# Performance work log

Measured on AMD Instinct MI355X. Metric: run time of the kernel, lower is better.

Reference implementation:

```python
import jax, jax.numpy as jnp
import numpy as np

B, M, K, N = 4, 2048, 4096, 4096


def setup_inputs() -> dict:
    key = jax.random.key(0)
    k1, k2, k3, k4, k5 = jax.random.split(key, 5)
    # quantized activations in [-8, 7], stored as int8 (spec dtype int32, cast here)
    x_q = jax.random.randint(k1, (B, M, K), -8, 8, dtype=jnp.int32).astype(jnp.int8)
    # per-token activation scales (B, M, 1)
    scales_x = jax.random.uniform(k2, (B, M, 1), dtype=jnp.float32, minval=0.001, maxval=0.02)
    # int8 weight (N, K) in [-8, 7] as produced by from_float
    weight = jax.random.randint(k3, (N, K), -8, 8, dtype=jnp.int32).astype(jnp.int8)
    # per-output-row weight scales (N, 1)
    weight_scales = jax.random.uniform(k4, (N, 1), dtype=jnp.float32, minval=0.001, maxval=0.02)
    bias = jax.random.normal(k5, (N,), dtype=jnp.float32) * 0.02
    return {"x_q": x_q, "scales_x": scales_x, "weight": weight,
            "weight_scales": weight_scales, "bias": bias}


def reference(x_q, scales_x, weight, weight_scales, bias):
    acc = jnp.einsum('bmk,nk->bmn', x_q, weight,
                     preferred_element_type=jnp.int32)  # (B, M, N) int32
    # sym_dequant: per-token scale * per-row weight scale, then fused bias add
    out = acc.astype(jnp.float32) * scales_x * weight_scales.reshape(1, 1, N) + bias
    return out
```

## Files before the change

### kernel.cpp

```cpp
#include <hip/hip_runtime.h>
#include <stdint.h>

#define MROWS 8192
#define K_DIM 4096
#define N_DIM 4096
#define BM 256
#define BN 256
#define BK 64
#define KT (K_DIM / BK)
#define ABYTES (BM * BK)
#define TBYTES (2 * ABYTES)

#define X_ELEMS (MROWS * K_DIM)
#define W_ELEMS (N_DIM * K_DIM)

typedef __attribute__((ext_vector_type(4))) int   int4v;
typedef __attribute__((ext_vector_type(4))) float float4v;

#define GLOAD_LDS16(gptr, lptr)                                                   \
    __builtin_amdgcn_global_load_lds((const __attribute__((address_space(1))) void*)(gptr), \
                                     (__attribute__((address_space(3))) void*)(lptr), 16, 0, 0)

__device__ __forceinline__ int pack4(int4v v) {
    return (int)((unsigned)(v[0] & 0xFF)
               | ((unsigned)(v[1] & 0xFF) << 8)
               | ((unsigned)(v[2] & 0xFF) << 16)
               | ((unsigned)(v[3] & 0xFF) << 24));
}

__global__ __launch_bounds__(256) void pack_i32_to_i8(
    const int4v* __restrict__ src, int4v* __restrict__ dst, int n16)
{
    int i = blockIdx.x * blockDim.x + threadIdx.x;
    if (i >= n16) return;
    int4v a = src[4 * i + 0];
    int4v b = src[4 * i + 1];
    int4v c = src[4 * i + 2];
    int4v d = src[4 * i + 3];
    int4v r;
    r[0] = pack4(a); r[1] = pack4(b); r[2] = pack4(c); r[3] = pack4(d);
    dst[i] = r;
}

__global__ __launch_bounds__(512, 2) void i8gemm_dq_kernel(
    const int8_t* __restrict__ xq,
    const float*  __restrict__ sx,
    const int8_t* __restrict__ wt,
    const float*  __restrict__ ws,
    const float*  __restrict__ bias,
    float*        __restrict__ out)
{
    __shared__ __align__(16) int8_t lds8[4 * TBYTES];

    const int tid  = threadIdx.x;
    const int wave = tid >> 6;
    const int lane = tid & 63;
    const int wr   = wave >> 2;
    const int wcn  = wave & 3;

    const int bid = blockIdx.x;
    const int wg  = (bid & 7) * 64 + (bid >> 3);
    const int ct  = wg & 15;
    const int rt  = wg >> 4;

    const int srow = wave * 16 + (lane >> 2);
    const int scol = (((lane & 3) - ((lane >> 3) & 3)) & 3) * 16;
    const int8_t* gA0 = xq + (size_t)(rt * BM + srow) * K_DIM + scol;
    const int8_t* gA1 = gA0 + (size_t)128 * K_DIM;
    const int8_t* gB0 = wt + (size_t)(ct * BN + srow) * K_DIM + scol;
    const int8_t* gB1 = gB0 + (size_t)128 * K_DIM;
    const int dA0 = wave * 1024;
    const int dA1 = 8192 + wave * 1024;
    const int dB0 = ABYTES + wave * 1024;
    const int dB1 = ABYTES + 8192 + wave * 1024;

    const int mrow = lane & 15;
    const int kswz = (((lane >> 4) + (mrow >> 1)) & 3) * 16;
    const int aoff = (wr * 128 + mrow) * BK + kswz;
    const int boff = ABYTES + (wcn * 64 + mrow) * BK + kswz;

    int4v acc[8][4] = {};

    #pragma unroll
    for (int u = 0; u < 3; ++u) {
        const size_t ko = (size_t)u * BK;
        int8_t* bb = lds8 + u * TBYTES;
        GLOAD_LDS16(gA0 + ko, bb + dA0);
        GLOAD_LDS16(gA1 + ko, bb + dA1);
        GLOAD_LDS16(gB0 + ko, bb + dB0);
        GLOAD_LDS16(gB1 + ko, bb + dB1);
    }

    #pragma unroll 4
    for (int t = 0; t < KT; ++t) {
        const int  buf = t & 3;
        const int  nb  = (t + 3) & 3;
        const int  u   = (t + 3) & (KT - 1);
        const size_t ko = (size_t)u * BK;
        const int8_t* base = lds8 + buf * TBYTES;
        int8_t* nbb = lds8 + nb * TBYTES;

        asm volatile("s_waitcnt vmcnt(8)" ::: "memory");
        __builtin_amdgcn_s_barrier();
        __builtin_amdgcn_sched_barrier(0);

        int4v a[4], b[4];
        #pragma unroll
        for (int i = 0; i < 4; ++i) a[i] = *(const int4v*)(base + aoff + i * 1024);
        #pragma unroll
        for (int j = 0; j < 4; ++j) b[j] = *(const int4v*)(base + boff + j * 1024);
        GLOAD_LDS16(gA0 + ko, nbb + dA0);
        GLOAD_LDS16(gA1 + ko, nbb + dA1);

        __builtin_amdgcn_s_setprio(1);
        #pragma unroll
        for (int i = 0; i < 4; ++i)
            #pragma unroll
            for (int j = 0; j < 4; ++j)
                acc[i][j] = __builtin_amdgcn_mfma_i32_16x16x64_i8(
                                a[i], b[j], acc[i][j], 0, 0, 0);
        __builtin_amdgcn_s_setprio(0);

        int4v a2[4];
        #pragma unroll
        for (int i = 0; i < 4; ++i) a2[i] = *(const int4v*)(base + aoff + (4 + i) * 1024);
        GLOAD_LDS16(gB0 + ko, nbb + dB0);
        GLOAD_LDS16(gB1 + ko, nbb + dB1);

        __builtin_amdgcn_s_setprio(1);
        #pragma unroll
        for (int i = 0; i < 4; ++i)
            #pragma unroll
            for (int j = 0; j < 4; ++j)
                acc[4 + i][j] = __builtin_amdgcn_mfma_i32_16x16x64_i8(
                                    a2[i], b[j], acc[4 + i][j], 0, 0, 0);
        __builtin_amdgcn_s_setprio(0);
    }

    asm volatile("s_waitcnt vmcnt(0)" ::: "memory");

    const int row_base = rt * BM + wr * 128;
    const int col_base = ct * BN + wcn * 64;
    const int crow = (lane >> 4) * 4;
    const int ccol = lane & 15;

    float wsc[4], bsc[4];
    #pragma unroll
    for (int j = 0; j < 4; ++j) {
        const int c = col_base + j * 16 + ccol;
        wsc[j] = ws[c];
        bsc[j] = bias[c];
    }

    #pragma unroll
    for (int i = 0; i < 8; ++i) {
        const int r0 = row_base + i * 16 + crow;
        const float4v sx4 = *(const float4v*)(sx + r0);
        #pragma unroll
        for (int j = 0; j < 4; ++j) {
            const int c = col_base + j * 16 + ccol;
            float* o = out + (size_t)r0 * N_DIM + c;
            #pragma unroll
            for (int r = 0; r < 4; ++r)
                o[(size_t)r * N_DIM] = (float)acc[i][j][r] * sx4[r] * wsc[j] + bsc[j];
        }
    }
}

extern "C" void kernel_launch(void* const* d_in, const int* in_sizes, int n_in,
                              void* d_out, int out_size, void* d_ws, size_t ws_size,
                              hipStream_t stream) {
    const int*   xq32 = (const int*)d_in[0];
    const float* sx   = (const float*)d_in[1];
    const int*   wt32 = (const int*)d_in[2];
    const float* ws   = (const float*)d_in[3];
    const float* bias = (const float*)d_in[4];
    float* out = (float*)d_out;

    int8_t* xq8 = (int8_t*)d_ws;
    int8_t* wt8 = xq8 + (size_t)X_ELEMS;

    {
        int n16x = X_ELEMS / 16;
        int n16w = W_ELEMS / 16;
        pack_i32_to_i8<<<n16x / 256, 256, 0, stream>>>((const int4v*)xq32, (int4v*)xq8, n16x);
        pack_i32_to_i8<<<n16w / 256, 256, 0, stream>>>((const int4v*)wt32, (int4v*)wt8, n16w);
    }

    dim3 grid((MROWS / BM) * (N_DIM / BN));
    i8gemm_dq_kernel<<<grid, 512, 0, stream>>>(xq8, sx, wt8, ws, bias, out);
}
```

Before: 396.4 us.

## Shrink GEMM tile to 256x128 with 4 waves and triple-buffered LDS

Halves the N tile to 128 and the workgroup to 4 waves, so the grid doubles and each wave keeps its 128x64 accumulator footprint. The LDS pipeline goes from 4 slots with 3 tiles in flight to 3 slots with 2 in flight. The loop now stops issuing prefetches for the last two K tiles, which are handled in a separate epilogue instead of wrapping around. The intent is smaller LDS use and better occupancy and load balance across CUs, at the cost of less reuse of A per workgroup and a shallower prefetch depth.

Result: slower. 410.0 us (+3.4%).

```diff
diff --git a/kernel.cpp b/kernel.cpp
--- a/kernel.cpp
+++ b/kernel.cpp
@@ -5,11 +5,12 @@
 #define K_DIM 4096
 #define N_DIM 4096
 #define BM 256
-#define BN 256
+#define BN 128
 #define BK 64
 #define KT (K_DIM / BK)
-#define ABYTES (BM * BK)
-#define TBYTES (2 * ABYTES)
+#define A_BYTES (BM * BK)
+#define B_BYTES (BN * BK)
+#define SLOT (A_BYTES + B_BYTES)
 
 #define X_ELEMS (MROWS * K_DIM)
 #define W_ELEMS (N_DIM * K_DIM)
@@ -42,7 +43,7 @@
     dst[i] = r;
 }
 
-__global__ __launch_bounds__(512, 2) void i8gemm_dq_kernel(
+__global__ __launch_bounds__(256, 2) void i8gemm_dq_kernel(
     const int8_t* __restrict__ xq,
     const float*  __restrict__ sx,
     const int8_t* __restrict__ wt,
@@ -50,57 +51,59 @@
     const float*  __restrict__ bias,
     float*        __restrict__ out)
 {
-    __shared__ __align__(16) int8_t lds8[4 * TBYTES];
+    __shared__ __align__(16) int8_t lds8[3 * SLOT];
 
     const int tid  = threadIdx.x;
     const int wave = tid >> 6;
     const int lane = tid & 63;
-    const int wr   = wave >> 2;
-    const int wcn  = wave & 3;
+    const int wrow = wave >> 1;
+    const int wcol = wave & 1;
 
     const int bid = blockIdx.x;
-    const int wg  = (bid & 7) * 64 + (bid >> 3);
-    const int ct  = wg & 15;
-    const int rt  = wg >> 4;
+    const int wg  = (bid & 7) * 128 + (bid >> 3);
+    const int ct  = wg & 31;
+    const int rt  = wg >> 5;
 
     const int srow = wave * 16 + (lane >> 2);
     const int scol = (((lane & 3) - ((lane >> 3) & 3)) & 3) * 16;
-    const int8_t* gA0 = xq + (size_t)(rt * BM + srow) * K_DIM + scol;
-    const int8_t* gA1 = gA0 + (size_t)128 * K_DIM;
-    const int8_t* gB0 = wt + (size_t)(ct * BN + srow) * K_DIM + scol;
-    const int8_t* gB1 = gB0 + (size_t)128 * K_DIM;
-    const int dA0 = wave * 1024;
-    const int dA1 = 8192 + wave * 1024;
-    const int dB0 = ABYTES + wave * 1024;
-    const int dB1 = ABYTES + 8192 + wave * 1024;
+    const int8_t* gA = xq + (size_t)(rt * BM + srow) * K_DIM + scol;
+    const int8_t* gB = wt + (size_t)(ct * BN + srow) * K_DIM + scol;
+    const int dA = wave * 1024;
+    const int dB = A_BYTES + wave * 1024;
 
     const int mrow = lane & 15;
     const int kswz = (((lane >> 4) + (mrow >> 1)) & 3) * 16;
-    const int aoff = (wr * 128 + mrow) * BK + kswz;
-    const int boff = ABYTES + (wcn * 64 + mrow) * BK + kswz;
+    const int aoff = (wrow * 128 + mrow) * BK + kswz;
+    const int boff = A_BYTES + (wcol * 64 + mrow) * BK + kswz;
 
     int4v acc[8][4] = {};
 
-    #pragma unroll
-    for (int u = 0; u < 3; ++u) {
-        const size_t ko = (size_t)u * BK;
-        int8_t* bb = lds8 + u * TBYTES;
-        GLOAD_LDS16(gA0 + ko, bb + dA0);
-        GLOAD_LDS16(gA1 + ko, bb + dA1);
-        GLOAD_LDS16(gB0 + ko, bb + dB0);
-        GLOAD_LDS16(gB1 + ko, bb + dB1);
-    }
-
-    #pragma unroll 4
-    for (int t = 0; t < KT; ++t) {
-        const int  buf = t & 3;
-        const int  nb  = (t + 3) & 3;
-        const int  u   = (t + 3) & (KT - 1);
-        const size_t ko = (size_t)u * BK;
-        const int8_t* base = lds8 + buf * TBYTES;
-        int8_t* nbb = lds8 + nb * TBYTES;
-
-        asm volatile("s_waitcnt vmcnt(8)" ::: "memory");
+#define STAGE_A012(U, S)                                       \
+    {                                                          \
+        const size_t ko_ = (size_t)(U) * BK;                   \
+        int8_t* bb_ = lds8 + (S) * SLOT;                       \
+        GLOAD_LDS16(gA + ko_,                   bb_ + dA);     \
+        GLOAD_LDS16(gA +  64 * K_DIM + ko_, bb_ + dA + 4096);  \
+        GLOAD_LDS16(gA + 128 * K_DIM + ko_, bb_ + dA + 8192);  \
+    }
+#define STAGE_A3B(U, S)                                        \
+    {                                                          \
+        const size_t ko_ = (size_t)(U) * BK;                   \
+        int8_t* bb_ = lds8 + (S) * SLOT;                       \
+        GLOAD_LDS16(gA + 192 * K_DIM + ko_, bb_ + dA + 12288); \
+        GLOAD_LDS16(gB + ko_,                   bb_ + dB);     \
+        GLOAD_LDS16(gB +  64 * K_DIM + ko_, bb_ + dB + 4096);  \
+    }
+
+    STAGE_A012(0, 0); STAGE_A3B(0, 0);
+    STAGE_A012(1, 1); STAGE_A3B(1, 1);
+
+    #pragma unroll 3
+    for (int t = 0; t < KT - 2; ++t) {
+        const int8_t* base = lds8 + (t % 3) * SLOT;
+        const int s2 = (t + 2) % 3;
+
+        asm volatile("s_waitcnt vmcnt(6)" ::: "memory");
         __builtin_amdgcn_s_barrier();
         __builtin_amdgcn_sched_barrier(0);
 
@@ -109,8 +112,7 @@
         for (int i = 0; i < 4; ++i) a[i] = *(const int4v*)(base + aoff + i * 1024);
         #pragma unroll
         for (int j = 0; j < 4; ++j) b[j] = *(const int4v*)(base + boff + j * 1024);
-        GLOAD_LDS16(gA0 + ko, nbb + dA0);
-        GLOAD_LDS16(gA1 + ko, nbb + dA1);
+        STAGE_A012(t + 2, s2);
 
         __builtin_amdgcn_s_setprio(1);
         #pragma unroll
@@ -124,8 +126,7 @@
         int4v a2[4];
         #pragma unroll
         for (int i = 0; i < 4; ++i) a2[i] = *(const int4v*)(base + aoff + (4 + i) * 1024);
-        GLOAD_LDS16(gB0 + ko, nbb + dB0);
-        GLOAD_LDS16(gB1 + ko, nbb + dB1);
+        STAGE_A3B(t + 2, s2);
 
         __builtin_amdgcn_s_setprio(1);
         #pragma unroll
@@ -137,10 +138,42 @@
         __builtin_amdgcn_s_setprio(0);
     }
 
-    asm volatile("s_waitcnt vmcnt(0)" ::: "memory");
-
-    const int row_base = rt * BM + wr * 128;
-    const int col_base = ct * BN + wcn * 64;
+    #pragma unroll
+    for (int e = 0; e < 2; ++e) {
+        const int t = KT - 2 + e;
+        const int8_t* base = lds8 + (t % 3) * SLOT;
+        if (e == 0) asm volatile("s_waitcnt vmcnt(6)" ::: "memory");
+        else        asm volatile("s_waitcnt vmcnt(0)" ::: "memory");
+        __builtin_amdgcn_s_barrier();
+        __builtin_amdgcn_sched_barrier(0);
+        int4v a[4], b[4], a2[4];
+        #pragma unroll
+        for (int i = 0; i < 4; ++i) a[i]  = *(const int4v*)(base + aoff + i * 1024);
+        #pragma unroll
+        for (int j = 0; j < 4; ++j) b[j]  = *(const int4v*)(base + boff + j * 1024);
+        #pragma unroll
+        for (int i = 0; i < 4; ++i) a2[i] = *(const int4v*)(base + aoff + (4 + i) * 1024);
+        __builtin_amdgcn_s_setprio(1);
+        #pragma unroll
+        for (int i = 0; i < 4; ++i)
+            #pragma unroll
+            for (int j = 0; j < 4; ++j)
+                acc[i][j] = __builtin_amdgcn_mfma_i32_16x16x64_i8(
+                                a[i], b[j], acc[i][j], 0, 0, 0);
+        #pragma unroll
+        for (int i = 0; i < 4; ++i)
+            #pragma unroll
+            for (int j = 0; j < 4; ++j)
+                acc[4 + i][j] = __builtin_amdgcn_mfma_i32_16x16x64_i8(
+                                    a2[i], b[j], acc[4 + i][j], 0, 0, 0);
+        __builtin_amdgcn_s_setprio(0);
+    }
+
+#undef STAGE_A012
+#undef STAGE_A3B
+
+    const int row_base = rt * BM + wrow * 128;
+    const int col_base = ct * BN + wcol * 64;
     const int crow = (lane >> 4) * 4;
     const int ccol = lane & 15;
 
@@ -188,5 +221,5 @@
     }
 
     dim3 grid((MROWS / BM) * (N_DIM / BN));
-    i8gemm_dq_kernel<<<grid, 512, 0, stream>>>(xq8, sx, wt8, ws, bias, out);
-}
+    i8gemm_dq_kernel<<<grid, 256, 0, stream>>>(xq8, sx, wt8, ws, bias, out);
+}
```
